# Optimization experiments

Measured on AMD Instinct MI355X. Metric: run time of the kernel, lower is better.

## Reference

```python
import jax, jax.numpy as jnp
from jax import lax
import numpy as np

B, N, C = 4, 2000, 80           # images, proposals/img, foreground classes
SCORE_THR = 0.05
IOU_THR = 0.5
MAX_PER_IMG = 100
K_PRE = 2000                     # pre-NMS top-k candidates per image
STDS = np.array([0.1, 0.1, 0.2, 0.2], dtype=np.float32)
MAX_RATIO = float(abs(np.log(16.0 / 1000.0)))  # wh_ratio_clip=16/1000


def setup_inputs() -> dict:
    key = jax.random.key(0)
    k1, k2, k3 = jax.random.split(key, 3)
    class_outs = jax.random.normal(k1, (B, N, C + 1), dtype=jnp.float32)
    regression_outs = jax.random.normal(k2, (B, N, C * 4), dtype=jnp.float32) * 0.5
    # random valid proposal boxes inside 800x1333 images (x1<x2, y1<y2)
    xy = jax.random.uniform(k3, (B, N, 2, 2), dtype=jnp.float32)
    xy = xy * jnp.array([1333.0, 800.0], dtype=jnp.float32)
    lo = jnp.min(xy, axis=2)
    hi = jnp.max(xy, axis=2) + 1.0
    boxes = jnp.concatenate([lo, hi], axis=-1)  # [B,N,4] x1,y1,x2,y2
    images_hw = jnp.tile(jnp.array([[800, 1333]], dtype=jnp.int32), (B, 1))
    return {"class_outs": class_outs, "regression_outs": regression_outs,
            "boxes": boxes, "images_hw": images_hw}


def _decode(props, deltas, h, w):
    # props [N,4], deltas [N,C,4] -> decoded boxes [N,C,4], clipped to image
    d = deltas * jnp.asarray(STDS)
    dx, dy, dw, dh = d[..., 0], d[..., 1], d[..., 2], d[..., 3]
    dw = jnp.clip(dw, -MAX_RATIO, MAX_RATIO)
    dh = jnp.clip(dh, -MAX_RATIO, MAX_RATIO)
    px = (props[:, None, 0] + props[:, None, 2]) * 0.5
    py = (props[:, None, 1] + props[:, None, 3]) * 0.5
    pw = props[:, None, 2] - props[:, None, 0]
    ph = props[:, None, 3] - props[:, None, 1]
    gx = px + pw * dx
    gy = py + ph * dy
    gw = pw * jnp.exp(dw)
    gh = ph * jnp.exp(dh)
    x1 = jnp.clip(gx - gw * 0.5, 0.0, w)
    y1 = jnp.clip(gy - gh * 0.5, 0.0, h)
    x2 = jnp.clip(gx + gw * 0.5, 0.0, w)
    y2 = jnp.clip(gy + gh * 0.5, 0.0, h)
    return jnp.stack([x1, y1, x2, y2], axis=-1)


def _pairwise_iou(b):
    # b [K,4] -> iou [K,K]
    area = (b[:, 2] - b[:, 0]) * (b[:, 3] - b[:, 1])
    lt = jnp.maximum(b[:, None, :2], b[None, :, :2])
    rb = jnp.minimum(b[:, None, 2:], b[None, :, 2:])
    wh = jnp.clip(rb - lt, 0.0)
    inter = wh[..., 0] * wh[..., 1]
    return inter / (area[:, None] + area[None, :] - inter + 1e-6)


def _process_image(cls_out, reg_out, props, hw):
    h = hw[0].astype(jnp.float32)
    w = hw[1].astype(jnp.float32)
    scores = jax.nn.softmax(cls_out, axis=-1)[:, :C]          # drop background col
    bboxes = _decode(props, reg_out.reshape(N, C, 4), h, w)   # [N,C,4]
    flat_scores = scores.reshape(-1)                          # [N*C]
    flat_boxes = bboxes.reshape(-1, 4)
    labels = jnp.tile(jnp.arange(C, dtype=jnp.int32), N)      # class fastest-varying
    cand = jnp.where(flat_scores > SCORE_THR, flat_scores, -1.0)
    top_scores, top_idx = lax.top_k(cand, K_PRE)
    top_boxes = flat_boxes[top_idx]
    top_labels = labels[top_idx]
    valid = top_scores > SCORE_THR
    # class-offset trick: boxes of distinct classes never overlap
    off = top_labels.astype(jnp.float32)[:, None] * (jnp.maximum(h, w) + 1.0)
    iou = _pairwise_iou(top_boxes + off)                      # [K_PRE,K_PRE]
    idxs = jnp.arange(K_PRE)

    def body(i, keep):
        sup = (idxs > i) & (iou[i] > IOU_THR) & keep[i]
        return keep & ~sup

    keep = lax.fori_loop(0, K_PRE, body, valid)
    kept_scores = jnp.where(keep, top_scores, -1.0)
    det_scores, det_i = lax.top_k(kept_scores, MAX_PER_IMG)
    det_valid = det_scores > SCORE_THR
    det_boxes = jnp.where(det_valid[:, None], top_boxes[det_i], 0.0)
    det_labels = jnp.where(det_valid, top_labels[det_i], -1)
    det_scores = jnp.where(det_valid, det_scores, 0.0)
    return det_boxes, det_scores, det_labels


def reference(class_outs, regression_outs, boxes, images_hw):
    det_boxes, det_scores, det_labels = jax.vmap(_process_image)(
        class_outs, regression_outs, boxes, images_hw)
    return det_boxes, det_scores, det_labels
```

## Files before the change

### kernel.cpp

```cpp
#include <hip/hip_runtime.h>


typedef unsigned long long u64;
typedef unsigned int u32;

#define B_ 4
#define N_ 2000
#define C_ 80
#define NCLS 81
#define KPRE 2000
#define MAXDET 100
#define TARGET 256
#define NB 2312
#define NBPAD 2368
#define NG 37
#define HBASE 0xF500
#define KSHIFT 46
#define CAPA 320
#define CAPB 2048
#define NWAVE 16
#define SEGW 384
#define CAPBLK 128
#define BPI 125
#define BIGI 0x7fffffff

__device__ __forceinline__ u64 pack_key(float score, unsigned fi) {
  return ((u64)__float_as_uint(score) << 32) | (u64)(0xFFFFFFFFu - fi);
}

__device__ __forceinline__ float wred_max(float v) {
  int t;
#define STEPM(ctrl)                                                          \
  t = __builtin_amdgcn_update_dpp(__float_as_int(v), __float_as_int(v),      \
                                  (ctrl), 0xF, 0xF, false);                  \
  v = fmaxf(v, __int_as_float(t));
  STEPM(0x111) STEPM(0x112) STEPM(0x114) STEPM(0x118) STEPM(0x142) STEPM(0x143)
#undef STEPM
  return __int_as_float(__builtin_amdgcn_readlane(__float_as_int(v), 63));
}
__device__ __forceinline__ float wred_sum(float v) {
  int t;
#define STEPS(ctrl)                                                          \
  t = __builtin_amdgcn_update_dpp(0, __float_as_int(v), (ctrl), 0xF, 0xF,    \
                                  false);                                    \
  v = v + __int_as_float(t);
  STEPS(0x111) STEPS(0x112) STEPS(0x114) STEPS(0x118) STEPS(0x142) STEPS(0x143)
#undef STEPS
  return __int_as_float(__builtin_amdgcn_readlane(__float_as_int(v), 63));
}

__device__ __forceinline__ int dpp_min8(int v) {
  int t;
  t = __builtin_amdgcn_update_dpp(BIGI, v, 0x104, 0xF, 0xF, false);
  v = min(v, t);
  t = __builtin_amdgcn_update_dpp(BIGI, v, 0x102, 0xF, 0xF, false);
  v = min(v, t);
  t = __builtin_amdgcn_update_dpp(BIGI, v, 0x101, 0xF, 0xF, false);
  v = min(v, t);
  return v;
}

__device__ __forceinline__ float4 decode_one(
    u64 kk, const float* __restrict__ reg, const float* __restrict__ props,
    int b, float h, float w, float offscale) {
  const float MAXR = 4.135166556742356f;
  unsigned fi = 0xFFFFFFFFu - (u32)kk;
  int n = (int)(fi / (unsigned)C_);
  int c = (int)(fi - (unsigned)n * (unsigned)C_);
  float4 p = ((const float4*)props)[b * N_ + n];
  const float* dl = reg + ((size_t)(b * N_ + n)) * (C_ * 4) + c * 4;
  float dx = dl[0] * 0.1f;
  float dy = dl[1] * 0.1f;
  float dw = fminf(fmaxf(dl[2] * 0.2f, -MAXR), MAXR);
  float dh = fminf(fmaxf(dl[3] * 0.2f, -MAXR), MAXR);
  float px = (p.x + p.z) * 0.5f, py = (p.y + p.w) * 0.5f;
  float pw = p.z - p.x, ph = p.w - p.y;
  float gx = px + pw * dx, gy = py + ph * dy;
  float gw = pw * expf(dw), gh = ph * expf(dh);
  float off = (float)c * offscale;
  return make_float4(fminf(fmaxf(gx - gw * 0.5f, 0.0f), w) + off,
                     fminf(fmaxf(gy - gh * 0.5f, 0.0f), h) + off,
                     fminf(fmaxf(gx + gw * 0.5f, 0.0f), w) + off,
                     fminf(fmaxf(gy + gh * 0.5f, 0.0f), h) + off);
}

__global__ __launch_bounds__(1024) void cand_kernel(
    const float* __restrict__ cls, u64* __restrict__ gkeys, int* __restrict__ gcnt) {
  __shared__ int s_wc[16], s_woff[16];
  const int tid = threadIdx.x;
  const int w = tid >> 6, lane = tid & 63;
  const int blk = blockIdx.x;
  const int b = blk / BPI;
  const int n = (blk % BPI) * 16 + w;
  const float* lg = cls + (size_t)(b * N_ + n) * NCLS;
  float x0 = lg[lane];
  float x1 = (lane < 17) ? lg[64 + lane] : -3.0e38f;
  float mx = wred_max(fmaxf(x0, x1));
  float e0 = expf(x0 - mx);
  float e1 = (lane < 17) ? expf(x1 - mx) : 0.0f;
  float sum = wred_sum(e0 + e1);
  float sc0 = e0 / sum, sc1 = e1 / sum;
  bool p0 = sc0 > 0.05f;
  bool p1 = (lane < 16) && (sc1 > 0.05f);
  u64 m0 = __ballot(p0), m1 = __ballot(p1);
  int c0 = __popcll(m0);
  if (lane == 0) s_wc[w] = c0 + __popcll(m1);
  __syncthreads();
  if (tid == 0) {
    int acc = 0;
#pragma unroll
    for (int i = 0; i < 16; ++i) { s_woff[i] = acc; acc += s_wc[i]; }
    gcnt[blk] = acc;
  }
  __syncthreads();
  const int base = s_woff[w];
  const u64 lt = (1ull << lane) - 1;
  u64* gk = gkeys + (size_t)blk * CAPBLK;
  if (p0) {
    int slot = base + __popcll(m0 & lt);
    if (slot < CAPBLK) gk[slot] = pack_key(sc0, (unsigned)(n * C_ + lane));
  }
  if (p1) {
    int slot = base + c0 + __popcll(m1 & lt);
    if (slot < CAPBLK) gk[slot] = pack_key(sc1, (unsigned)(n * C_ + 64 + lane));
  }
}

__global__ __launch_bounds__(1024) void nmsA_kernel(
    const float* __restrict__ reg, const float* __restrict__ props,
    const int* __restrict__ hw, const u64* __restrict__ gkeys,
    const int* __restrict__ gcnt, int* __restrict__ gflag,
    float* __restrict__ out) {
  __shared__ u64 lds8[7952];
  char* bp = (char*)lds8;
  u64* keylist = (u64*)bp;
  u64* SS = (u64*)bp;
  u64* rb = (u64*)(bp + 8192);
  u32* hist = (u32*)(bp + 49152);
  float4* bxA = (float4*)(bp + 49152);
  u64* U = (u64*)(bp + 58624);
  int* outl = (int*)(bp + 62720);
  int* misc = (int*)(bp + 63232);
  int* segc = (int*)(bp + 63296);
  int* s_coarse = (int*)(bp + 63360);

  const int b = blockIdx.x, tid = threadIdx.x;
  const int wv = tid >> 6, lane = tid & 63;

  float h = (float)hw[b * 2 + 0];
  float w = (float)hw[b * 2 + 1];
  float offscale = fmaxf(h, w) + 1.0f;

  if (tid < 16) misc[tid] = 0;
  if (tid < 64) s_coarse[tid] = 0;
  for (int i = tid; i < NBPAD; i += 1024) hist[i] = 0;
  __syncthreads();

  {
    int cnts[8];
#pragma unroll
    for (int k = 0; k < 8; k++) {
      int p = wv + 16 * k;
      cnts[k] = (p < BPI) ? gcnt[b * BPI + p] : 0;
    }
    bool ovf = false;
    int segoff = 0;
#pragma unroll
    for (int k = 0; k < 8; k++) {
      int p = wv + 16 * k;
      if (p >= BPI) break;
      int cnt = cnts[k];
      if (cnt > CAPBLK) { ovf = true; cnt = CAPBLK; }
      const u64* seg = gkeys + (size_t)(b * BPI + p) * CAPBLK;
#pragma unroll
      for (int r = 0; r < 2; r++) {
        int idx = lane + 64 * r;
        if (idx < cnt) {
          u64 key = seg[idx];
          int bi = min(max((int)(key >> KSHIFT) - HBASE, 0), NB - 1);
          atomicAdd(&hist[bi], 1u);
          int slot = segoff + idx;
          if (slot < SEGW) keylist[wv * SEGW + slot] = key;
        }
      }
      segoff += cnt;
    }
    if (segoff > SEGW) ovf = true;
    if (lane == 0) {
      segc[wv] = min(segoff, SEGW);
      if (ovf) misc[7] = 1;
    }
  }
  __syncthreads();

  for (int g2 = wv; g2 < NG; g2 += NWAVE) {
    int v = (int)hist[(g2 << 6) | lane];
#pragma unroll
    for (int o = 32; o; o >>= 1) v += __shfl_xor(v, o);
    if (lane == 0) s_coarse[g2] = v;
  }
  __syncthreads();

  if (tid < 64) {
    int v = s_coarse[lane];
#pragma unroll
    for (int off = 1; off < 64; off <<= 1) {
      int src = lane + off;
      int o = __shfl(v, src < 64 ? src : 63);
      if (src < 64) v += o;
    }
    int Mtot = __shfl(v, 0);
    u64 pm = __ballot(v >= TARGET);
    int T_A = 0, S_A;
    if (pm) {
      int gs = 63 - __builtin_clzll(pm);
      int beyond = __shfl(v, gs + 1);
      int fv = (int)hist[(gs << 6) | lane];
#pragma unroll
      for (int off = 1; off < 64; off <<= 1) {
        int src = lane + off;
        int o = __shfl(fv, src < 64 ? src : 63);
        if (src < 64) fv += o;
      }
      int cum = beyond + fv;
      u64 pm2 = __ballot(cum >= TARGET);
      int tr = 63 - __builtin_clzll(pm2);
      T_A = (gs << 6) + tr;
      S_A = __shfl(cum, tr);
    } else {
      S_A = Mtot;
    }
    if (lane == 0) { misc[0] = T_A; misc[2] = S_A; misc[3] = Mtot; misc[4] = 0; }
  }
  __syncthreads();

  int T_A = misc[0], S_A = misc[2], Mtot = misc[3];
  bool modeB = (S_A > CAPA) || (misc[7] != 0);
  int K = 0, nkept = 0;

  if (!modeB) {
    for (int s = 0; s < NWAVE; s++) {
      int Mg = segc[s];
      bool pred = false;
      u64 key = 0;
      if (tid < Mg) {
        key = keylist[s * SEGW + tid];
        int bi = min(max((int)(key >> KSHIFT) - HBASE, 0), NB - 1);
        pred = (bi >= T_A);
      }
      u64 mk = __ballot(pred);
      if (mk) {
        int wbase = 0;
        if (lane == 0) wbase = atomicAdd(&misc[4], __popcll(mk));
        wbase = __shfl(wbase, 0);
        if (pred) {
          int pos = wbase + __popcll(mk & ((1ull << lane) - 1));
          if (pos < CAPA) U[pos] = key;
        }
      }
    }
    __syncthreads();
    int S = misc[4];
    if (S > CAPA) S = CAPA;
    if (tid == 0 && (S & 1)) U[S] = 0ULL;
    __syncthreads();
    if (tid < S) {
      u64 k1 = U[tid];
      int r1 = 0;
      const ulonglong2* Uu2 = (const ulonglong2*)U;
      int half = (S + 1) >> 1;
      for (int k = 0; k < half; k++) {
        ulonglong2 kk = Uu2[k];
        r1 += (kk.x > k1) + (kk.y > k1);
      }
      SS[r1] = k1;
    }
    __syncthreads();
    K = S;
    for (int j = tid; j < K; j += 1024)
      bxA[j] = decode_one(SS[j], reg, props, b, h, w, offscale);
    __syncthreads();

    int nwords = (S + 63) >> 6;
    int ntiles = nwords * (nwords + 1) / 2;
    for (int t = wv; t < ntiles; t += NWAVE) {
      int ti = 0, rem = t;
      while (rem >= nwords - ti) { rem -= nwords - ti; ti++; }
      int tj = ti + rem;
      int i = (ti << 6) + lane;
      float4 bi4 = bxA[i];
      float ai = (bi4.z - bi4.x) * (bi4.w - bi4.y);
      u64 bits = 0;
      int jbase = tj << 6;
      int jcount = min(64, S - jbase);
      for (int jj = 0; jj < jcount; jj++) {
        int j = jbase + jj;
        float4 bj = bxA[j];
        float aj = (bj.z - bj.x) * (bj.w - bj.y);
        float iw = fmaxf(fminf(bi4.z, bj.z) - fmaxf(bi4.x, bj.x), 0.0f);
        float ih = fmaxf(fminf(bi4.w, bj.w) - fmaxf(bi4.y, bj.y), 0.0f);
        float inter = iw * ih;
        float iou = inter / (ai + aj - inter + 1e-6f);
        if (j > i && iou > 0.5f) bits |= (1ull << jj);
      }
      if (i < S) rb[i * 8 + tj] = bits;
    }
    __syncthreads();

    if (tid < 64) {
      u64 alive = 0;
      if (lane < nwords) {
        alive = ~0ull;
        int remb = S & 63;
        if (lane == nwords - 1 && remb) alive = (1ull << remb) - 1;
      }
      int nk = 0;
      if (S > 0) {
        int i = 0;
        u64 row = (lane < nwords) ? rb[0 * 8 + lane] : 0ull;
        for (;;) {
          if (lane == 0) outl[nk] = i;
          nk++;
          if (nk >= MAXDET) break;
          if (lane == (i >> 6)) alive &= ~(1ull << (i & 63));
          u64 rowSpec = (i + 1 < S && lane < nwords) ? rb[(i + 1) * 8 + lane] : 0ull;
          u64 a2 = alive & ~row;
          alive = a2;
          int cnd = a2 ? ((lane << 6) + (int)__builtin_ctzll(a2)) : BIGI;
          int m8 = dpp_min8(cnd);
          int ni = __builtin_amdgcn_readfirstlane(m8);
          if (ni >= BIGI) break;
          row = (ni == i + 1) ? rowSpec
                              : ((lane < nwords) ? rb[ni * 8 + lane] : 0ull);
          i = ni;
        }
      }
      if (lane == 0) misc[6] = nk;
    }
    __syncthreads();
    nkept = misc[6];
    if (nkept < MAXDET && K < Mtot && K < KPRE) modeB = true;
  }

  if (tid == 0) gflag[b] = modeB ? 1 : 0;
  if (modeB) return;

  float* oBox = out;
  float* oSc = out + B_ * MAXDET * 4;
  float* oLb = out + B_ * MAXDET * 5;
  for (int k2 = tid; k2 < MAXDET; k2 += 1024) {
    float4 bb = make_float4(0.0f, 0.0f, 0.0f, 0.0f);
    float sv = 0.0f, lv = -1.0f;
    if (k2 < nkept) {
      int idx = outl[k2];
      u64 kk = SS[idx];
      sv = __uint_as_float((u32)(kk >> 32));
      unsigned fi = 0xFFFFFFFFu - (u32)kk;
      int c = (int)(fi % (unsigned)C_);
      float off = (float)c * offscale;
      float4 ob = bxA[idx];
      bb = make_float4(ob.x - off, ob.y - off, ob.z - off, ob.w - off);
      lv = (float)c;
    }
    oBox[(b * MAXDET + k2) * 4 + 0] = bb.x;
    oBox[(b * MAXDET + k2) * 4 + 1] = bb.y;
    oBox[(b * MAXDET + k2) * 4 + 2] = bb.z;
    oBox[(b * MAXDET + k2) * 4 + 3] = bb.w;
    oSc[b * MAXDET + k2] = sv;
    oLb[b * MAXDET + k2] = lv;
  }
}

__global__ __launch_bounds__(1024) void nmsB_kernel(
    const float* __restrict__ reg, const float* __restrict__ props,
    const int* __restrict__ hw, const u64* __restrict__ gkeys,
    const int* __restrict__ gcnt, const int* __restrict__ gflag,
    float* __restrict__ out) {
  const int b = blockIdx.x, tid = threadIdx.x;
  if (gflag[b] == 0) return;

  __shared__ u64 lds8[7952];
  char* bp = (char*)lds8;
  u32* hist = (u32*)(bp + 0);
  u64* U2 = (u64*)(bp + 9472);
  u64* SSB = (u64*)(bp + 25856);
  int* outl = (int*)(bp + 42240);
  int* misc = (int*)(bp + 42752);
  const int wv = tid >> 6, lane = tid & 63;

  float h = (float)hw[b * 2 + 0];
  float w = (float)hw[b * 2 + 1];
  float offscale = fmaxf(h, w) + 1.0f;

  for (int i = tid; i < NBPAD; i += 1024) hist[i] = 0;
  if (tid < 16) misc[tid] = 0;
  __syncthreads();

  for (int k = 0; k < 8; k++) {
    int p = wv + 16 * k;
    if (p >= BPI) break;
    int cnt = min(gcnt[b * BPI + p], CAPBLK);
    const u64* seg = gkeys + (size_t)(b * BPI + p) * CAPBLK;
#pragma unroll
    for (int r = 0; r < 2; r++) {
      int idx = lane + 64 * r;
      if (idx < cnt) {
        u64 key = seg[idx];
        int bi = min(max((int)(key >> KSHIFT) - HBASE, 0), NB - 1);
        atomicAdd(&hist[bi], 1u);
      }
    }
  }
  __syncthreads();

  if (tid == 0) {
    int acc = 0, tb = 0;
    for (int bi = NB - 1; bi >= 0; bi--) {
      acc += (int)hist[bi];
      if (acc >= KPRE) { tb = bi; break; }
    }
    if (acc > CAPB) tb = min(tb + 1, NB - 1);
    misc[1] = tb;
    misc[4] = 0;
  }
  __syncthreads();
  int T_B = misc[1];

  for (int k = 0; k < 8; k++) {
    int p = wv + 16 * k;
    if (p >= BPI) break;
    int cnt = min(gcnt[b * BPI + p], CAPBLK);
    const u64* seg = gkeys + (size_t)(b * BPI + p) * CAPBLK;
#pragma unroll
    for (int r = 0; r < 2; r++) {
      int idx = lane + 64 * r;
      bool pred = false;
      u64 key = 0;
      if (idx < cnt) {
        key = seg[idx];
        int bi = min(max((int)(key >> KSHIFT) - HBASE, 0), NB - 1);
        pred = (bi >= T_B);
      }
      u64 mk = __ballot(pred);
      if (mk) {
        int wbase = 0;
        if (lane == 0) wbase = atomicAdd(&misc[4], __popcll(mk));
        wbase = __shfl(wbase, 0);
        if (pred) {
          int pos = wbase + __popcll(mk & ((1ull << lane) - 1));
          if (pos < CAPB) U2[pos] = key;
        }
      }
    }
  }
  __syncthreads();
  int S = misc[4];
  if (S > CAPB) S = CAPB;
  {
    int j1 = tid, j2 = tid + 1024;
    u64 k1 = (j1 < S) ? U2[j1] : 0ULL;
    u64 k2 = (j2 < S) ? U2[j2] : 0ULL;
    int r1 = 0, r2 = 0;
    for (int k = 0; k < S; k++) {
      u64 kk = U2[k];
// ... 51 lines not shown
      i = ni;
    }
  }
  if (tid == 0) misc[6] = nk;
  __syncthreads();
  int nkept = misc[6];

  float* oBox = out;
  float* oSc = out + B_ * MAXDET * 4;
  float* oLb = out + B_ * MAXDET * 5;
  for (int k2 = tid; k2 < MAXDET; k2 += 1024) {
    float4 bb = make_float4(0.0f, 0.0f, 0.0f, 0.0f);
    float sv = 0.0f, lv = -1.0f;
    if (k2 < nkept) {
      int idx = outl[k2];
      u64 kk = SSB[idx];
      sv = __uint_as_float((u32)(kk >> 32));
      unsigned fi = 0xFFFFFFFFu - (u32)kk;
      int c = (int)(fi % (unsigned)C_);
      float off = (float)c * offscale;
      float4 ob = decode_one(kk, reg, props, b, h, w, offscale);
      bb = make_float4(ob.x - off, ob.y - off, ob.z - off, ob.w - off);
      lv = (float)c;
    }
    oBox[(b * MAXDET + k2) * 4 + 0] = bb.x;
    oBox[(b * MAXDET + k2) * 4 + 1] = bb.y;
    oBox[(b * MAXDET + k2) * 4 + 2] = bb.z;
    oBox[(b * MAXDET + k2) * 4 + 3] = bb.w;
    oSc[b * MAXDET + k2] = sv;
    oLb[b * MAXDET + k2] = lv;
  }
}

extern "C" void kernel_launch(void* const* d_in, const int* in_sizes, int n_in,
                              void* d_out, int out_size, void* d_ws, size_t ws_size,
                              hipStream_t stream) {
  const float* cls = (const float*)d_in[0];
  const float* reg = (const float*)d_in[1];
  const float* props = (const float*)d_in[2];
  const int* hw = (const int*)d_in[3];
  float* out = (float*)d_out;

  int* gcnt = (int*)d_ws;
  u64* gkeys = (u64*)((char*)d_ws + 2048);
  int* gflag = (int*)((char*)d_ws + 514048);

  cand_kernel<<<B_ * BPI, 1024, 0, stream>>>(cls, gkeys, gcnt);
  nmsA_kernel<<<B_, 1024, 0, stream>>>(reg, props, hw, gkeys, gcnt, gflag, out);
  nmsB_kernel<<<B_, 1024, 0, stream>>>(reg, props, hw, gkeys, gcnt, gflag, out);
}
```

Baseline: 107.1 us.

## Fuse candidate, NMS-A and NMS-B kernels into one launch with flag spin-wait

Merges the candidate-scoring kernel and both NMS kernels into a single launch. Every block writes its candidate keys and then publishes its count with a magic-tagged release store. The first B blocks go on to do NMS, spin-waiting with acquire loads on each producer's flag, and call a noinline cold path instead of a separate fallback kernel. This removes two kernel launches and their gaps. The risks are inter-block spin dependencies that rely on all blocks being scheduled, and tagged flags left in the workspace from earlier calls that are never cleared, so a later call may read stale counts.

```diff
diff --git a/kernel.cpp b/kernel.cpp
--- a/kernel.cpp
+++ b/kernel.cpp
@@ -23,6 +23,7 @@
 #define CAPBLK 128
 #define BPI 125
 #define BIGI 0x7fffffff
+#define MAGIC 0x5EC7u
 
 __device__ __forceinline__ u64 pack_key(float score, unsigned fi) {
   return ((u64)__float_as_uint(score) << 32) | (u64)(0xFFFFFFFFu - fi);
@@ -84,313 +85,17 @@
                      fminf(fmaxf(gy + gh * 0.5f, 0.0f), h) + off);
 }
 
-__global__ __launch_bounds__(1024) void cand_kernel(
-    const float* __restrict__ cls, u64* __restrict__ gkeys, int* __restrict__ gcnt) {
-  __shared__ int s_wc[16], s_woff[16];
-  const int tid = threadIdx.x;
-  const int w = tid >> 6, lane = tid & 63;
-  const int blk = blockIdx.x;
-  const int b = blk / BPI;
-  const int n = (blk % BPI) * 16 + w;
-  const float* lg = cls + (size_t)(b * N_ + n) * NCLS;
-  float x0 = lg[lane];
-  float x1 = (lane < 17) ? lg[64 + lane] : -3.0e38f;
-  float mx = wred_max(fmaxf(x0, x1));
-  float e0 = expf(x0 - mx);
-  float e1 = (lane < 17) ? expf(x1 - mx) : 0.0f;
-  float sum = wred_sum(e0 + e1);
-  float sc0 = e0 / sum, sc1 = e1 / sum;
-  bool p0 = sc0 > 0.05f;
-  bool p1 = (lane < 16) && (sc1 > 0.05f);
-  u64 m0 = __ballot(p0), m1 = __ballot(p1);
-  int c0 = __popcll(m0);
-  if (lane == 0) s_wc[w] = c0 + __popcll(m1);
-  __syncthreads();
-  if (tid == 0) {
-    int acc = 0;
-#pragma unroll
-    for (int i = 0; i < 16; ++i) { s_woff[i] = acc; acc += s_wc[i]; }
-    gcnt[blk] = acc;
-  }
-  __syncthreads();
-  const int base = s_woff[w];
-  const u64 lt = (1ull << lane) - 1;
-  u64* gk = gkeys + (size_t)blk * CAPBLK;
-  if (p0) {
-    int slot = base + __popcll(m0 & lt);
-    if (slot < CAPBLK) gk[slot] = pack_key(sc0, (unsigned)(n * C_ + lane));
-  }
-  if (p1) {
-    int slot = base + c0 + __popcll(m1 & lt);
-    if (slot < CAPBLK) gk[slot] = pack_key(sc1, (unsigned)(n * C_ + 64 + lane));
-  }
-}
-
-__global__ __launch_bounds__(1024) void nmsA_kernel(
-    const float* __restrict__ reg, const float* __restrict__ props,
-    const int* __restrict__ hw, const u64* __restrict__ gkeys,
-    const int* __restrict__ gcnt, int* __restrict__ gflag,
-    float* __restrict__ out) {
-  __shared__ u64 lds8[7952];
-  char* bp = (char*)lds8;
-  u64* keylist = (u64*)bp;
-  u64* SS = (u64*)bp;
-  u64* rb = (u64*)(bp + 8192);
-  u32* hist = (u32*)(bp + 49152);
-  float4* bxA = (float4*)(bp + 49152);
-  u64* U = (u64*)(bp + 58624);
-  int* outl = (int*)(bp + 62720);
-  int* misc = (int*)(bp + 63232);
-  int* segc = (int*)(bp + 63296);
-  int* s_coarse = (int*)(bp + 63360);
-
-  const int b = blockIdx.x, tid = threadIdx.x;
-  const int wv = tid >> 6, lane = tid & 63;
-
-  float h = (float)hw[b * 2 + 0];
-  float w = (float)hw[b * 2 + 1];
-  float offscale = fmaxf(h, w) + 1.0f;
-
-  if (tid < 16) misc[tid] = 0;
-  if (tid < 64) s_coarse[tid] = 0;
-  for (int i = tid; i < NBPAD; i += 1024) hist[i] = 0;
-  __syncthreads();
-
-  {
-    int cnts[8];
-#pragma unroll
-    for (int k = 0; k < 8; k++) {
-      int p = wv + 16 * k;
-      cnts[k] = (p < BPI) ? gcnt[b * BPI + p] : 0;
-    }
-    bool ovf = false;
-    int segoff = 0;
-#pragma unroll
-    for (int k = 0; k < 8; k++) {
-      int p = wv + 16 * k;
-      if (p >= BPI) break;
-      int cnt = cnts[k];
-      if (cnt > CAPBLK) { ovf = true; cnt = CAPBLK; }
-      const u64* seg = gkeys + (size_t)(b * BPI + p) * CAPBLK;
-#pragma unroll
-      for (int r = 0; r < 2; r++) {
-        int idx = lane + 64 * r;
-        if (idx < cnt) {
-          u64 key = seg[idx];
-          int bi = min(max((int)(key >> KSHIFT) - HBASE, 0), NB - 1);
-          atomicAdd(&hist[bi], 1u);
-          int slot = segoff + idx;
-          if (slot < SEGW) keylist[wv * SEGW + slot] = key;
-        }
-      }
-      segoff += cnt;
-    }
-    if (segoff > SEGW) ovf = true;
-    if (lane == 0) {
-      segc[wv] = min(segoff, SEGW);
-      if (ovf) misc[7] = 1;
-    }
-  }
-  __syncthreads();
-
-  for (int g2 = wv; g2 < NG; g2 += NWAVE) {
-    int v = (int)hist[(g2 << 6) | lane];
-#pragma unroll
-    for (int o = 32; o; o >>= 1) v += __shfl_xor(v, o);
-    if (lane == 0) s_coarse[g2] = v;
-  }
-  __syncthreads();
-
-  if (tid < 64) {
-    int v = s_coarse[lane];
-#pragma unroll
-    for (int off = 1; off < 64; off <<= 1) {
-      int src = lane + off;
-      int o = __shfl(v, src < 64 ? src : 63);
-      if (src < 64) v += o;
-    }
-    int Mtot = __shfl(v, 0);
-    u64 pm = __ballot(v >= TARGET);
-    int T_A = 0, S_A;
-    if (pm) {
-      int gs = 63 - __builtin_clzll(pm);
-      int beyond = __shfl(v, gs + 1);
-      int fv = (int)hist[(gs << 6) | lane];
-#pragma unroll
-      for (int off = 1; off < 64; off <<= 1) {
-        int src = lane + off;
-        int o = __shfl(fv, src < 64 ? src : 63);
-        if (src < 64) fv += o;
-      }
-      int cum = beyond + fv;
-      u64 pm2 = __ballot(cum >= TARGET);
-      int tr = 63 - __builtin_clzll(pm2);
-      T_A = (gs << 6) + tr;
-      S_A = __shfl(cum, tr);
-    } else {
-      S_A = Mtot;
-    }
-    if (lane == 0) { misc[0] = T_A; misc[2] = S_A; misc[3] = Mtot; misc[4] = 0; }
-  }
-  __syncthreads();
-
-  int T_A = misc[0], S_A = misc[2], Mtot = misc[3];
-  bool modeB = (S_A > CAPA) || (misc[7] != 0);
-  int K = 0, nkept = 0;
-
-  if (!modeB) {
-    for (int s = 0; s < NWAVE; s++) {
-      int Mg = segc[s];
-      bool pred = false;
-      u64 key = 0;
-      if (tid < Mg) {
-        key = keylist[s * SEGW + tid];
-        int bi = min(max((int)(key >> KSHIFT) - HBASE, 0), NB - 1);
-        pred = (bi >= T_A);
-      }
-      u64 mk = __ballot(pred);
-      if (mk) {
-        int wbase = 0;
-        if (lane == 0) wbase = atomicAdd(&misc[4], __popcll(mk));
-        wbase = __shfl(wbase, 0);
-        if (pred) {
-          int pos = wbase + __popcll(mk & ((1ull << lane) - 1));
-          if (pos < CAPA) U[pos] = key;
-        }
-      }
-    }
-    __syncthreads();
-    int S = misc[4];
-    if (S > CAPA) S = CAPA;
-    if (tid == 0 && (S & 1)) U[S] = 0ULL;
-    __syncthreads();
-    if (tid < S) {
-      u64 k1 = U[tid];
-      int r1 = 0;
-      const ulonglong2* Uu2 = (const ulonglong2*)U;
-      int half = (S + 1) >> 1;
-      for (int k = 0; k < half; k++) {
-        ulonglong2 kk = Uu2[k];
-        r1 += (kk.x > k1) + (kk.y > k1);
-      }
-      SS[r1] = k1;
-    }
-    __syncthreads();
-    K = S;
-    for (int j = tid; j < K; j += 1024)
-      bxA[j] = decode_one(SS[j], reg, props, b, h, w, offscale);
-    __syncthreads();
-
-    int nwords = (S + 63) >> 6;
-    int ntiles = nwords * (nwords + 1) / 2;
-    for (int t = wv; t < ntiles; t += NWAVE) {
-      int ti = 0, rem = t;
-      while (rem >= nwords - ti) { rem -= nwords - ti; ti++; }
-      int tj = ti + rem;
-      int i = (ti << 6) + lane;
-      float4 bi4 = bxA[i];
-      float ai = (bi4.z - bi4.x) * (bi4.w - bi4.y);
-      u64 bits = 0;
-      int jbase = tj << 6;
-      int jcount = min(64, S - jbase);
-      for (int jj = 0; jj < jcount; jj++) {
-        int j = jbase + jj;
-        float4 bj = bxA[j];
-        float aj = (bj.z - bj.x) * (bj.w - bj.y);
-        float iw = fmaxf(fminf(bi4.z, bj.z) - fmaxf(bi4.x, bj.x), 0.0f);
-        float ih = fmaxf(fminf(bi4.w, bj.w) - fmaxf(bi4.y, bj.y), 0.0f);
-        float inter = iw * ih;
-        float iou = inter / (ai + aj - inter + 1e-6f);
-        if (j > i && iou > 0.5f) bits |= (1ull << jj);
-      }
-      if (i < S) rb[i * 8 + tj] = bits;
-    }
-    __syncthreads();
-
-    if (tid < 64) {
-      u64 alive = 0;
-      if (lane < nwords) {
-        alive = ~0ull;
-        int remb = S & 63;
-        if (lane == nwords - 1 && remb) alive = (1ull << remb) - 1;
-      }
-      int nk = 0;
-      if (S > 0) {
-        int i = 0;
-        u64 row = (lane < nwords) ? rb[0 * 8 + lane] : 0ull;
-        for (;;) {
-          if (lane == 0) outl[nk] = i;
-          nk++;
-          if (nk >= MAXDET) break;
-          if (lane == (i >> 6)) alive &= ~(1ull << (i & 63));
-          u64 rowSpec = (i + 1 < S && lane < nwords) ? rb[(i + 1) * 8 + lane] : 0ull;
-          u64 a2 = alive & ~row;
-          alive = a2;
-          int cnd = a2 ? ((lane << 6) + (int)__builtin_ctzll(a2)) : BIGI;
-          int m8 = dpp_min8(cnd);
-          int ni = __builtin_amdgcn_readfirstlane(m8);
-          if (ni >= BIGI) break;
-          row = (ni == i + 1) ? rowSpec
-                              : ((lane < nwords) ? rb[ni * 8 + lane] : 0ull);
-          i = ni;
-        }
-      }
-      if (lane == 0) misc[6] = nk;
-    }
-    __syncthreads();
-    nkept = misc[6];
-    if (nkept < MAXDET && K < Mtot && K < KPRE) modeB = true;
-  }
-
-  if (tid == 0) gflag[b] = modeB ? 1 : 0;
-  if (modeB) return;
-
-  float* oBox = out;
-  float* oSc = out + B_ * MAXDET * 4;
-  float* oLb = out + B_ * MAXDET * 5;
-  for (int k2 = tid; k2 < MAXDET; k2 += 1024) {
-    float4 bb = make_float4(0.0f, 0.0f, 0.0f, 0.0f);
-    float sv = 0.0f, lv = -1.0f;
-    if (k2 < nkept) {
-      int idx = outl[k2];
-      u64 kk = SS[idx];
-      sv = __uint_as_float((u32)(kk >> 32));
-      unsigned fi = 0xFFFFFFFFu - (u32)kk;
-      int c = (int)(fi % (unsigned)C_);
-      float off = (float)c * offscale;
-      float4 ob = bxA[idx];
-      bb = make_float4(ob.x - off, ob.y - off, ob.z - off, ob.w - off);
-      lv = (float)c;
-    }
-    oBox[(b * MAXDET + k2) * 4 + 0] = bb.x;
-    oBox[(b * MAXDET + k2) * 4 + 1] = bb.y;
-    oBox[(b * MAXDET + k2) * 4 + 2] = bb.z;
-    oBox[(b * MAXDET + k2) * 4 + 3] = bb.w;
-    oSc[b * MAXDET + k2] = sv;
-    oLb[b * MAXDET + k2] = lv;
-  }
-}
-
-__global__ __launch_bounds__(1024) void nmsB_kernel(
-    const float* __restrict__ reg, const float* __restrict__ props,
-    const int* __restrict__ hw, const u64* __restrict__ gkeys,
-    const int* __restrict__ gcnt, const int* __restrict__ gflag,
-    float* __restrict__ out) {
-  const int b = blockIdx.x, tid = threadIdx.x;
-  if (gflag[b] == 0) return;
-
-  __shared__ u64 lds8[7952];
-  char* bp = (char*)lds8;
+__device__ __noinline__ static void nmsB_cold(
+    char* bp, const float* __restrict__ reg, const float* __restrict__ props,
+    const u64* __restrict__ gkeys, const u32* __restrict__ gcnt,
+    float* __restrict__ out, int b, float h, float w, float offscale) {
   u32* hist = (u32*)(bp + 0);
   u64* U2 = (u64*)(bp + 9472);
   u64* SSB = (u64*)(bp + 25856);
   int* outl = (int*)(bp + 42240);
   int* misc = (int*)(bp + 42752);
+  const int tid = threadIdx.x;
   const int wv = tid >> 6, lane = tid & 63;
-
-  float h = (float)hw[b * 2 + 0];
-  float w = (float)hw[b * 2 + 1];
-  float offscale = fmaxf(h, w) + 1.0f;
 
   for (int i = tid; i < NBPAD; i += 1024) hist[i] = 0;
   if (tid < 16) misc[tid] = 0;
@@ -399,7 +104,7 @@
   for (int k = 0; k < 8; k++) {
     int p = wv + 16 * k;
     if (p >= BPI) break;
-    int cnt = min(gcnt[b * BPI + p], CAPBLK);
+    int cnt = min((int)(gcnt[b * BPI + p] & 0xFFFFu), CAPBLK);
     const u64* seg = gkeys + (size_t)(b * BPI + p) * CAPBLK;
 #pragma unroll
     for (int r = 0; r < 2; r++) {
@@ -429,7 +134,7 @@
   for (int k = 0; k < 8; k++) {
     int p = wv + 16 * k;
     if (p >= BPI) break;
-    int cnt = min(gcnt[b * BPI + p], CAPBLK);
+    int cnt = min((int)(gcnt[b * BPI + p] & 0xFFFFu), CAPBLK);
     const u64* seg = gkeys + (size_t)(b * BPI + p) * CAPBLK;
 #pragma unroll
     for (int r = 0; r < 2; r++) {
@@ -547,6 +252,303 @@
   }
 }
 
+__global__ __launch_bounds__(1024) void fused_kernel(
+    const float* __restrict__ cls, const float* __restrict__ reg,
+    const float* __restrict__ props, const int* __restrict__ hw,
+    u64* __restrict__ gkeys, u32* __restrict__ gcnt, float* __restrict__ out) {
+  __shared__ u64 lds8[7976];
+  char* bp = (char*)lds8;
+  u64* keylist = (u64*)bp;
+  u64* SS = (u64*)bp;
+  u64* rb = (u64*)(bp + 8192);
+  u32* hist = (u32*)(bp + 49152);
+  float4* bxA = (float4*)(bp + 49152);
+  u64* U = (u64*)(bp + 58624);
+  int* outl = (int*)(bp + 62720);
+  int* misc = (int*)(bp + 63232);
+  int* segc = (int*)(bp + 63296);
+  int* s_coarse = (int*)(bp + 63360);
+  int* s_wc = (int*)(bp + 63616);
+  int* s_woff = (int*)(bp + 63680);
+
+  const int tid = threadIdx.x;
+  const int wv = tid >> 6, lane = tid & 63;
+
+  {
+    const int blk = blockIdx.x;
+    const int pb = blk / BPI;
+    const int n = (blk % BPI) * 16 + wv;
+    const float* lg = cls + (size_t)(pb * N_ + n) * NCLS;
+    float x0 = lg[lane];
+    float x1 = (lane < 17) ? lg[64 + lane] : -3.0e38f;
+    float mx = wred_max(fmaxf(x0, x1));
+    float e0 = expf(x0 - mx);
+    float e1 = (lane < 17) ? expf(x1 - mx) : 0.0f;
+    float sum = wred_sum(e0 + e1);
+    float sc0 = e0 / sum, sc1 = e1 / sum;
+    bool p0 = sc0 > 0.05f;
+    bool p1 = (lane < 16) && (sc1 > 0.05f);
+    u64 m0 = __ballot(p0), m1 = __ballot(p1);
+    int c0 = __popcll(m0);
+    if (lane == 0) s_wc[wv] = c0 + __popcll(m1);
+    __syncthreads();
+    int acc_keep = 0;
+    if (tid == 0) {
+      int acc = 0;
+#pragma unroll
+      for (int i = 0; i < 16; ++i) { s_woff[i] = acc; acc += s_wc[i]; }
+      acc_keep = acc;
+    }
+    __syncthreads();
+    const int base = s_woff[wv];
+    const u64 lt = (1ull << lane) - 1;
+    u64* gk = gkeys + (size_t)blk * CAPBLK;
+    if (p0) {
+      int slot = base + __popcll(m0 & lt);
+      if (slot < CAPBLK) gk[slot] = pack_key(sc0, (unsigned)(n * C_ + lane));
+    }
+    if (p1) {
+      int slot = base + c0 + __popcll(m1 & lt);
+      if (slot < CAPBLK) gk[slot] = pack_key(sc1, (unsigned)(n * C_ + 64 + lane));
+    }
+    __syncthreads();
+    if (tid == 0) {
+      __threadfence();
+      __hip_atomic_store(&gcnt[blk], (u32)acc_keep | (MAGIC << 16),
+                         __ATOMIC_RELEASE, __HIP_MEMORY_SCOPE_AGENT);
+    }
+  }
+
+  const int b = blockIdx.x;
+  if (b >= B_) return;
+
+  if (tid < 16) misc[tid] = 0;
+  if (tid < 64) s_coarse[tid] = 0;
+  for (int i = tid; i < NBPAD; i += 1024) hist[i] = 0;
+  float h = (float)hw[b * 2 + 0];
+  float w = (float)hw[b * 2 + 1];
+  float offscale = fmaxf(h, w) + 1.0f;
+  __syncthreads();
+
+  {
+    bool ovf = false;
+    int segoff = 0;
+    for (int k = 0; k < 8; k++) {
+      int p = wv + 16 * k;
+      if (p >= BPI) break;
+      u32 v = 0;
+      if (lane == 0) {
+        do {
+          v = __hip_atomic_load(&gcnt[b * BPI + p], __ATOMIC_ACQUIRE,
+                                __HIP_MEMORY_SCOPE_AGENT);
+        } while ((v >> 16) != MAGIC);
+      }
+      v = (u32)__shfl((int)v, 0);
+      int cnt = (int)(v & 0xFFFFu);
+      if (cnt > CAPBLK) { ovf = true; cnt = CAPBLK; }
+      const u64* seg = gkeys + (size_t)(b * BPI + p) * CAPBLK;
+#pragma unroll
+      for (int r = 0; r < 2; r++) {
+        int idx = lane + 64 * r;
+        if (idx < cnt) {
+          u64 key = seg[idx];
+          int bi = min(max((int)(key >> KSHIFT) - HBASE, 0), NB - 1);
+          atomicAdd(&hist[bi], 1u);
+          int slot = segoff + idx;
+          if (slot < SEGW) keylist[wv * SEGW + slot] = key;
+        }
+      }
+      segoff += cnt;
+    }
+    if (segoff > SEGW) ovf = true;
+    if (lane == 0) {
+      segc[wv] = min(segoff, SEGW);
+      if (ovf) misc[7] = 1;
+    }
+  }
+  __syncthreads();
+
+  for (int g2 = wv; g2 < NG; g2 += NWAVE) {
+    int v = (int)hist[(g2 << 6) | lane];
+#pragma unroll
+    for (int o = 32; o; o >>= 1) v += __shfl_xor(v, o);
+    if (lane == 0) s_coarse[g2] = v;
+  }
+  __syncthreads();
+
+  if (tid < 64) {
+    int v = s_coarse[lane];
+#pragma unroll
+    for (int off = 1; off < 64; off <<= 1) {
+      int src = lane + off;
+      int o = __shfl(v, src < 64 ? src : 63);
+      if (src < 64) v += o;
+    }
+    int Mtot = __shfl(v, 0);
+    u64 pm = __ballot(v >= TARGET);
+    int T_A = 0, S_A;
+    if (pm) {
+      int gs = 63 - __builtin_clzll(pm);
+      int beyond = __shfl(v, gs + 1);
+      int fv = (int)hist[(gs << 6) | lane];
+#pragma unroll
+      for (int off = 1; off < 64; off <<= 1) {
+        int src = lane + off;
+        int o = __shfl(fv, src < 64 ? src : 63);
+        if (src < 64) fv += o;
+      }
+      int cum = beyond + fv;
+      u64 pm2 = __ballot(cum >= TARGET);
+      int tr = 63 - __builtin_clzll(pm2);
+      T_A = (gs << 6) + tr;
+      S_A = __shfl(cum, tr);
+    } else {
+      S_A = Mtot;
+    }
+    if (lane == 0) { misc[0] = T_A; misc[2] = S_A; misc[3] = Mtot; misc[4] = 0; }
+  }
+  __syncthreads();
+
+  int T_A = misc[0], S_A = misc[2], Mtot = misc[3];
+  bool modeB = (S_A > CAPA) || (misc[7] != 0);
+  int K = 0, nkept = 0;
+
+  if (!modeB) {
+    for (int s = 0; s < NWAVE; s++) {
+      int Mg = segc[s];
+      bool pred = false;
+      u64 key = 0;
+      if (tid < Mg) {
+        key = keylist[s * SEGW + tid];
+        int bi = min(max((int)(key >> KSHIFT) - HBASE, 0), NB - 1);
+        pred = (bi >= T_A);
+      }
+      u64 mk = __ballot(pred);
+      if (mk) {
+        int wbase = 0;
+        if (lane == 0) wbase = atomicAdd(&misc[4], __popcll(mk));
+        wbase = __shfl(wbase, 0);
+        if (pred) {
+          int pos = wbase + __popcll(mk & ((1ull << lane) - 1));
+          if (pos < CAPA) U[pos] = key;
+        }
+      }
+    }
+    __syncthreads();
+    int S = misc[4];
+    if (S > CAPA) S = CAPA;
+    if (tid == 0 && (S & 1)) U[S] = 0ULL;
+    __syncthreads();
+    if (tid < S) {
+      u64 k1 = U[tid];
+      int r1 = 0;
+      const ulonglong2* Uu2 = (const ulonglong2*)U;
+      int half = (S + 1) >> 1;
+      for (int k = 0; k < half; k++) {
+        ulonglong2 kk = Uu2[k];
+        r1 += (kk.x > k1) + (kk.y > k1);
+      }
+      SS[r1] = k1;
+    }
+    __syncthreads();
+    K = S;
+    for (int j = tid; j < K; j += 1024)
+      bxA[j] = decode_one(SS[j], reg, props, b, h, w, offscale);
+    __syncthreads();
+
+    int nwords = (S + 63) >> 6;
+    int ntiles = nwords * (nwords + 1) / 2;
+    for (int t = wv; t < ntiles; t += NWAVE) {
+      int ti = 0, rem = t;
+      while (rem >= nwords - ti) { rem -= nwords - ti; ti++; }
+      int tj = ti + rem;
+      int i = (ti << 6) + lane;
+      float4 bi4 = bxA[i];
+      float ai = (bi4.z - bi4.x) * (bi4.w - bi4.y);
+      u64 bits = 0;
+      int jbase = tj << 6;
+      int jcount = min(64, S - jbase);
+      for (int jj = 0; jj < jcount; jj++) {
+        int j = jbase + jj;
+        float4 bj = bxA[j];
+        float aj = (bj.z - bj.x) * (bj.w - bj.y);
+        float iw = fmaxf(fminf(bi4.z, bj.z) - fmaxf(bi4.x, bj.x), 0.0f);
+        float ih = fmaxf(fminf(bi4.w, bj.w) - fmaxf(bi4.y, bj.y), 0.0f);
+        float inter = iw * ih;
+        float iou = inter / (ai + aj - inter + 1e-6f);
+        if (j > i && iou > 0.5f) bits |= (1ull << jj);
+      }
+      if (i < S) rb[i * 8 + tj] = bits;
+    }
+    __syncthreads();
+
+    if (tid < 64) {
+      int nwords7 = (S + 63) >> 6;
+      u64 alive = 0;
+      if (lane < nwords7) {
+        alive = ~0ull;
+        int remb = S & 63;
+        if (lane == nwords7 - 1 && remb) alive = (1ull << remb) - 1;
+      }
+      int nk = 0;
+      if (S > 0) {
+        int i = 0;
+        u64 row = (lane < nwords7) ? rb[0 * 8 + lane] : 0ull;
+        for (;;) {
+          if (lane == 0) outl[nk] = i;
+          nk++;
+          if (nk >= MAXDET) break;
+          if (lane == (i >> 6)) alive &= ~(1ull << (i & 63));
+          u64 rowSpec = (i + 1 < S && lane < nwords7) ? rb[(i + 1) * 8 + lane] : 0ull;
+          u64 a2 = alive & ~row;
+          alive = a2;
+          int cnd = a2 ? ((lane << 6) + (int)__builtin_ctzll(a2)) : BIGI;
+          int m8 = dpp_min8(cnd);
+          int ni = __builtin_amdgcn_readfirstlane(m8);
+          if (ni >= BIGI) break;
+          row = (ni == i + 1) ? rowSpec
+                              : ((lane < nwords7) ? rb[ni * 8 + lane] : 0ull);
+          i = ni;
+        }
+      }
+      if (lane == 0) misc[6] = nk;
+    }
+    __syncthreads();
+    nkept = misc[6];
+    if (nkept < MAXDET && K < Mtot && K < KPRE) modeB = true;
+  }
+
+  if (modeB) {
+    nmsB_cold(bp, reg, props, gkeys, gcnt, out, b, h, w, offscale);
+    return;
+  }
+
+  float* oBox = out;
+  float* oSc = out + B_ * MAXDET * 4;
+  float* oLb = out + B_ * MAXDET * 5;
+  for (int k2 = tid; k2 < MAXDET; k2 += 1024) {
+    float4 bb = make_float4(0.0f, 0.0f, 0.0f, 0.0f);
+    float sv = 0.0f, lv = -1.0f;
+    if (k2 < nkept) {
+      int idx = outl[k2];
+      u64 kk = SS[idx];
+      sv = __uint_as_float((u32)(kk >> 32));
+      unsigned fi = 0xFFFFFFFFu - (u32)kk;
+      int c = (int)(fi % (unsigned)C_);
+      float off = (float)c * offscale;
+      float4 ob = bxA[idx];
+      bb = make_float4(ob.x - off, ob.y - off, ob.z - off, ob.w - off);
+      lv = (float)c;
+    }
+    oBox[(b * MAXDET + k2) * 4 + 0] = bb.x;
+    oBox[(b * MAXDET + k2) * 4 + 1] = bb.y;
+    oBox[(b * MAXDET + k2) * 4 + 2] = bb.z;
+    oBox[(b * MAXDET + k2) * 4 + 3] = bb.w;
+    oSc[b * MAXDET + k2] = sv;
+    oLb[b * MAXDET + k2] = lv;
+  }
+}
+
 extern "C" void kernel_launch(void* const* d_in, const int* in_sizes, int n_in,
                               void* d_out, int out_size, void* d_ws, size_t ws_size,
                               hipStream_t stream) {
@@ -556,11 +558,9 @@
   const int* hw = (const int*)d_in[3];
   float* out = (float*)d_out;
 
-  int* gcnt = (int*)d_ws;
+  u32* gcnt = (u32*)d_ws;
   u64* gkeys = (u64*)((char*)d_ws + 2048);
-  int* gflag = (int*)((char*)d_ws + 514048);
-
-  cand_kernel<<<B_ * BPI, 1024, 0, stream>>>(cls, gkeys, gcnt);
-  nmsA_kernel<<<B_, 1024, 0, stream>>>(reg, props, hw, gkeys, gcnt, gflag, out);
-  nmsB_kernel<<<B_, 1024, 0, stream>>>(reg, props, hw, gkeys, gcnt, gflag, out);
-}
+
+  fused_kernel<<<B_ * BPI, 1024, 0, stream>>>(cls, reg, props, hw,
+                                              gkeys, gcnt, out);
+}
```

Result: slower. 134.5 us (+25.6%).

## Build score histogram in candidate kernel and split threshold into separate kernel

Applied to the files above, without the earlier changes.

The per-image score histogram is now built with global atomics inside the 500-block candidate kernel instead of being rebuilt inside the 4-block NMS kernel. A new small thresh_kernel turns that histogram into the top-k bucket threshold. nmsA then makes a single pass over the keys to filter them, with no staging keylist and a smaller shared-memory footprint. This moves serial work off the few-block NMS stage, at the cost of an extra memset, an extra kernel launch and contended global atomics.

```diff
diff --git a/kernel.cpp b/kernel.cpp
--- a/kernel.cpp
+++ b/kernel.cpp
@@ -18,14 +18,21 @@
 #define KSHIFT 46
 #define CAPA 320
 #define CAPB 2048
-#define NWAVE 16
-#define SEGW 384
 #define CAPBLK 128
 #define BPI 125
 #define BIGI 0x7fffffff
 
+#define WS_GCNT  0
+#define WS_GKEYS 2048
+#define WS_GFLAG 514048
+#define WS_GTHR  514064
+#define WS_GHIST 514112
+
 __device__ __forceinline__ u64 pack_key(float score, unsigned fi) {
   return ((u64)__float_as_uint(score) << 32) | (u64)(0xFFFFFFFFu - fi);
+}
+__device__ __forceinline__ int bucket_of_bits(u32 sb) {
+  return min(max((int)(sb >> 14) - HBASE, 0), NB - 1);
 }
 
 __device__ __forceinline__ float wred_max(float v) {
@@ -85,7 +92,8 @@
 }
 
 __global__ __launch_bounds__(1024) void cand_kernel(
-    const float* __restrict__ cls, u64* __restrict__ gkeys, int* __restrict__ gcnt) {
+    const float* __restrict__ cls, u64* __restrict__ gkeys,
+    int* __restrict__ gcnt, u32* __restrict__ ghist) {
   __shared__ int s_wc[16], s_woff[16];
   const int tid = threadIdx.x;
   const int w = tid >> 6, lane = tid & 63;
@@ -116,91 +124,35 @@
   const int base = s_woff[w];
   const u64 lt = (1ull << lane) - 1;
   u64* gk = gkeys + (size_t)blk * CAPBLK;
+  u32* gh = ghist + (size_t)b * NBPAD;
   if (p0) {
     int slot = base + __popcll(m0 & lt);
     if (slot < CAPBLK) gk[slot] = pack_key(sc0, (unsigned)(n * C_ + lane));
+    atomicAdd(&gh[bucket_of_bits(__float_as_uint(sc0))], 1u);
   }
   if (p1) {
     int slot = base + c0 + __popcll(m1 & lt);
     if (slot < CAPBLK) gk[slot] = pack_key(sc1, (unsigned)(n * C_ + 64 + lane));
-  }
-}
-
-__global__ __launch_bounds__(1024) void nmsA_kernel(
-    const float* __restrict__ reg, const float* __restrict__ props,
-    const int* __restrict__ hw, const u64* __restrict__ gkeys,
-    const int* __restrict__ gcnt, int* __restrict__ gflag,
-    float* __restrict__ out) {
-  __shared__ u64 lds8[7952];
-  char* bp = (char*)lds8;
-  u64* keylist = (u64*)bp;
-  u64* SS = (u64*)bp;
-  u64* rb = (u64*)(bp + 8192);
-  u32* hist = (u32*)(bp + 49152);
-  float4* bxA = (float4*)(bp + 49152);
-  u64* U = (u64*)(bp + 58624);
-  int* outl = (int*)(bp + 62720);
-  int* misc = (int*)(bp + 63232);
-  int* segc = (int*)(bp + 63296);
-  int* s_coarse = (int*)(bp + 63360);
-
+    atomicAdd(&gh[bucket_of_bits(__float_as_uint(sc1))], 1u);
+  }
+}
+
+__global__ __launch_bounds__(1024) void thresh_kernel(
+    const u32* __restrict__ ghist, int* __restrict__ gthr) {
+  __shared__ u32 hist[NBPAD];
+  __shared__ int s_coarse[64];
   const int b = blockIdx.x, tid = threadIdx.x;
   const int wv = tid >> 6, lane = tid & 63;
-
-  float h = (float)hw[b * 2 + 0];
-  float w = (float)hw[b * 2 + 1];
-  float offscale = fmaxf(h, w) + 1.0f;
-
-  if (tid < 16) misc[tid] = 0;
+  for (int i = tid; i < NBPAD; i += 1024) hist[i] = ghist[b * NBPAD + i];
   if (tid < 64) s_coarse[tid] = 0;
-  for (int i = tid; i < NBPAD; i += 1024) hist[i] = 0;
-  __syncthreads();
-
-  {
-    int cnts[8];
-#pragma unroll
-    for (int k = 0; k < 8; k++) {
-      int p = wv + 16 * k;
-      cnts[k] = (p < BPI) ? gcnt[b * BPI + p] : 0;
-    }
-    bool ovf = false;
-    int segoff = 0;
-#pragma unroll
-    for (int k = 0; k < 8; k++) {
-      int p = wv + 16 * k;
-      if (p >= BPI) break;
-      int cnt = cnts[k];
-      if (cnt > CAPBLK) { ovf = true; cnt = CAPBLK; }
-      const u64* seg = gkeys + (size_t)(b * BPI + p) * CAPBLK;
-#pragma unroll
-      for (int r = 0; r < 2; r++) {
-        int idx = lane + 64 * r;
-        if (idx < cnt) {
-          u64 key = seg[idx];
-          int bi = min(max((int)(key >> KSHIFT) - HBASE, 0), NB - 1);
-          atomicAdd(&hist[bi], 1u);
-          int slot = segoff + idx;
-          if (slot < SEGW) keylist[wv * SEGW + slot] = key;
-        }
-      }
-      segoff += cnt;
-    }
-    if (segoff > SEGW) ovf = true;
-    if (lane == 0) {
-      segc[wv] = min(segoff, SEGW);
-      if (ovf) misc[7] = 1;
-    }
-  }
-  __syncthreads();
-
-  for (int g2 = wv; g2 < NG; g2 += NWAVE) {
+  __syncthreads();
+  for (int g2 = wv; g2 < NG; g2 += 16) {
     int v = (int)hist[(g2 << 6) | lane];
 #pragma unroll
     for (int o = 32; o; o >>= 1) v += __shfl_xor(v, o);
     if (lane == 0) s_coarse[g2] = v;
   }
   __syncthreads();
-
   if (tid < 64) {
     int v = s_coarse[lane];
 #pragma unroll
@@ -230,116 +182,166 @@
     } else {
       S_A = Mtot;
     }
-    if (lane == 0) { misc[0] = T_A; misc[2] = S_A; misc[3] = Mtot; misc[4] = 0; }
-  }
-  __syncthreads();
-
-  int T_A = misc[0], S_A = misc[2], Mtot = misc[3];
-  bool modeB = (S_A > CAPA) || (misc[7] != 0);
+    if (lane == 0) {
+      gthr[b * 4 + 0] = T_A;
+      gthr[b * 4 + 1] = S_A;
+      gthr[b * 4 + 2] = Mtot;
+    }
+  }
+}
+
+__global__ __launch_bounds__(1024) void nmsA_kernel(
+    const float* __restrict__ reg, const float* __restrict__ props,
+    const int* __restrict__ hw, const u64* __restrict__ gkeys,
+    const int* __restrict__ gcnt, const int* __restrict__ gthr,
+    int* __restrict__ gflag, float* __restrict__ out) {
+  __shared__ u64 lds8[4106];
+  char* bp = (char*)lds8;
+  u64* SS = (u64*)bp;
+  u64* rb = (u64*)(bp + 4096);
+  float4* bxA = (float4*)(bp + 24576);
+  u64* U = (u64*)(bp + 29696);
+  int* outl = (int*)(bp + 32272);
+  int* misc = (int*)(bp + 32784);
+
+  const int b = blockIdx.x, tid = threadIdx.x;
+  const int wv = tid >> 6, lane = tid & 63;
+
+  float h = (float)hw[b * 2 + 0];
+  float w = (float)hw[b * 2 + 1];
+  float offscale = fmaxf(h, w) + 1.0f;
+  const int T_A = gthr[b * 4 + 0];
+  const int S_A = gthr[b * 4 + 1];
+  const int Mtot = gthr[b * 4 + 2];
+
+  if (tid < 16) misc[tid] = 0;
+  __syncthreads();
+
+  bool modeB = (S_A > CAPA);
   int K = 0, nkept = 0;
 
   if (!modeB) {
-    for (int s = 0; s < NWAVE; s++) {
-      int Mg = segc[s];
-      bool pred = false;
-      u64 key = 0;
-      if (tid < Mg) {
-        key = keylist[s * SEGW + tid];
-        int bi = min(max((int)(key >> KSHIFT) - HBASE, 0), NB - 1);
-        pred = (bi >= T_A);
-      }
-      u64 mk = __ballot(pred);
-      if (mk) {
-        int wbase = 0;
-        if (lane == 0) wbase = atomicAdd(&misc[4], __popcll(mk));
-        wbase = __shfl(wbase, 0);
-        if (pred) {
-          int pos = wbase + __popcll(mk & ((1ull << lane) - 1));
-          if (pos < CAPA) U[pos] = key;
-        }
-      }
-    }
+    int cnts[8];
+#pragma unroll
+    for (int k = 0; k < 8; k++) {
+      int p = wv + 16 * k;
+      cnts[k] = (p < BPI) ? gcnt[b * BPI + p] : 0;
+    }
+    bool ovf = false;
+#pragma unroll
+    for (int k = 0; k < 8; k++) {
+      int p = wv + 16 * k;
+      if (p >= BPI) break;
+      int cnt = cnts[k];
+      if (cnt > CAPBLK) { ovf = true; cnt = CAPBLK; }
+      const u64* seg = gkeys + (size_t)(b * BPI + p) * CAPBLK;
+#pragma unroll
+      for (int r = 0; r < 2; r++) {
+        int idx = lane + 64 * r;
+        bool pred = false;
+        u64 key = 0;
+        if (idx < cnt) {
+          key = seg[idx];
+          pred = (bucket_of_bits((u32)(key >> 32)) >= T_A);
+        }
+        u64 mk = __ballot(pred);
+        if (mk) {
+          int wbase = 0;
+          if (lane == 0) wbase = atomicAdd(&misc[4], __popcll(mk));
+          wbase = __shfl(wbase, 0);
+          if (pred) {
+            int pos = wbase + __popcll(mk & ((1ull << lane) - 1));
+            if (pos < CAPA) U[pos] = key;
+          }
+        }
+      }
+    }
+    if (lane == 0 && ovf) misc[7] = 1;
     __syncthreads();
+    if (misc[7]) modeB = true;
     int S = misc[4];
     if (S > CAPA) S = CAPA;
-    if (tid == 0 && (S & 1)) U[S] = 0ULL;
-    __syncthreads();
-    if (tid < S) {
-      u64 k1 = U[tid];
-      int r1 = 0;
-      const ulonglong2* Uu2 = (const ulonglong2*)U;
-      int half = (S + 1) >> 1;
-      for (int k = 0; k < half; k++) {
-        ulonglong2 kk = Uu2[k];
-        r1 += (kk.x > k1) + (kk.y > k1);
-      }
-      SS[r1] = k1;
-    }
-    __syncthreads();
-    K = S;
-    for (int j = tid; j < K; j += 1024)
-      bxA[j] = decode_one(SS[j], reg, props, b, h, w, offscale);
-    __syncthreads();
-
-    int nwords = (S + 63) >> 6;
-    int ntiles = nwords * (nwords + 1) / 2;
-    for (int t = wv; t < ntiles; t += NWAVE) {
-      int ti = 0, rem = t;
-      while (rem >= nwords - ti) { rem -= nwords - ti; ti++; }
-      int tj = ti + rem;
-      int i = (ti << 6) + lane;
-      float4 bi4 = bxA[i];
-      float ai = (bi4.z - bi4.x) * (bi4.w - bi4.y);
-      u64 bits = 0;
-      int jbase = tj << 6;
-      int jcount = min(64, S - jbase);
-      for (int jj = 0; jj < jcount; jj++) {
-        int j = jbase + jj;
-        float4 bj = bxA[j];
-        float aj = (bj.z - bj.x) * (bj.w - bj.y);
-        float iw = fmaxf(fminf(bi4.z, bj.z) - fmaxf(bi4.x, bj.x), 0.0f);
-        float ih = fmaxf(fminf(bi4.w, bj.w) - fmaxf(bi4.y, bj.y), 0.0f);
-        float inter = iw * ih;
-        float iou = inter / (ai + aj - inter + 1e-6f);
-        if (j > i && iou > 0.5f) bits |= (1ull << jj);
-      }
-      if (i < S) rb[i * 8 + tj] = bits;
-    }
-    __syncthreads();
-
-    if (tid < 64) {
-      u64 alive = 0;
-      if (lane < nwords) {
-        alive = ~0ull;
-        int remb = S & 63;
-        if (lane == nwords - 1 && remb) alive = (1ull << remb) - 1;
-      }
-      int nk = 0;
-      if (S > 0) {
-        int i = 0;
-        u64 row = (lane < nwords) ? rb[0 * 8 + lane] : 0ull;
-        for (;;) {
-          if (lane == 0) outl[nk] = i;
-          nk++;
-          if (nk >= MAXDET) break;
-          if (lane == (i >> 6)) alive &= ~(1ull << (i & 63));
-          u64 rowSpec = (i + 1 < S && lane < nwords) ? rb[(i + 1) * 8 + lane] : 0ull;
-          u64 a2 = alive & ~row;
-          alive = a2;
-          int cnd = a2 ? ((lane << 6) + (int)__builtin_ctzll(a2)) : BIGI;
-          int m8 = dpp_min8(cnd);
-          int ni = __builtin_amdgcn_readfirstlane(m8);
-          if (ni >= BIGI) break;
-          row = (ni == i + 1) ? rowSpec
-                              : ((lane < nwords) ? rb[ni * 8 + lane] : 0ull);
-          i = ni;
-        }
-      }
-      if (lane == 0) misc[6] = nk;
-    }
-    __syncthreads();
-    nkept = misc[6];
-    if (nkept < MAXDET && K < Mtot && K < KPRE) modeB = true;
+
+    if (!modeB) {
+      if (tid == 0 && (S & 1)) U[S] = 0ULL;
+      __syncthreads();
+      if (tid < S) {
+        u64 k1 = U[tid];
+        int r1 = 0;
+        const ulonglong2* Uu2 = (const ulonglong2*)U;
+        int half = (S + 1) >> 1;
+        for (int k = 0; k < half; k++) {
+          ulonglong2 kk = Uu2[k];
+          r1 += (kk.x > k1) + (kk.y > k1);
+        }
+        SS[r1] = k1;
+      }
+      __syncthreads();
+      K = S;
+      for (int j = tid; j < K; j += 1024)
+        bxA[j] = decode_one(SS[j], reg, props, b, h, w, offscale);
+      __syncthreads();
+
+      int nwords = (S + 63) >> 6;
+      int ntiles = nwords * (nwords + 1) / 2;
+      for (int t = wv; t < ntiles; t += 16) {
+        int ti = 0, rem = t;
+        while (rem >= nwords - ti) { rem -= nwords - ti; ti++; }
+        int tj = ti + rem;
+        int i = (ti << 6) + lane;
+        float4 bi4 = bxA[i];
+        float ai = (bi4.z - bi4.x) * (bi4.w - bi4.y);
+        u64 bits = 0;
+        int jbase = tj << 6;
+        int jcount = min(64, S - jbase);
+        for (int jj = 0; jj < jcount; jj++) {
+          int j = jbase + jj;
+          float4 bj = bxA[j];
+          float aj = (bj.z - bj.x) * (bj.w - bj.y);
+          float iw = fmaxf(fminf(bi4.z, bj.z) - fmaxf(bi4.x, bj.x), 0.0f);
+          float ih = fmaxf(fminf(bi4.w, bj.w) - fmaxf(bi4.y, bj.y), 0.0f);
+          float inter = iw * ih;
+          float iou = inter / (ai + aj - inter + 1e-6f);
+          if (j > i && iou > 0.5f) bits |= (1ull << jj);
+        }
+        if (i < S) rb[i * 8 + tj] = bits;
+      }
+      __syncthreads();
+
+      if (tid < 64) {
+        u64 alive = 0;
+        if (lane < nwords) {
+          alive = ~0ull;
+          int remb = S & 63;
+          if (lane == nwords - 1 && remb) alive = (1ull << remb) - 1;
+        }
+        int nk = 0;
+        if (S > 0) {
+          int i = 0;
+          u64 row = (lane < nwords) ? rb[0 * 8 + lane] : 0ull;
+          for (;;) {
+            if (lane == 0) outl[nk] = i;
+            nk++;
+            if (nk >= MAXDET) break;
+            if (lane == (i >> 6)) alive &= ~(1ull << (i & 63));
+            u64 rowSpec = (i + 1 < S && lane < nwords) ? rb[(i + 1) * 8 + lane] : 0ull;
+            u64 a2 = alive & ~row;
+            alive = a2;
+            int cnd = a2 ? ((lane << 6) + (int)__builtin_ctzll(a2)) : BIGI;
+            int m8 = dpp_min8(cnd);
+            int ni = __builtin_amdgcn_readfirstlane(m8);
+            if (ni >= BIGI) break;
+            row = (ni == i + 1) ? rowSpec
+                                : ((lane < nwords) ? rb[ni * 8 + lane] : 0ull);
+            i = ni;
+          }
+        }
+        if (lane == 0) misc[6] = nk;
+      }
+      __syncthreads();
+      nkept = misc[6];
+      if (nkept < MAXDET && K < Mtot && K < KPRE) modeB = true;
+    }
   }
 
   if (tid == 0) gflag[b] = modeB ? 1 : 0;
@@ -556,11 +558,16 @@
   const int* hw = (const int*)d_in[3];
   float* out = (float*)d_out;
 
-  int* gcnt = (int*)d_ws;
-  u64* gkeys = (u64*)((char*)d_ws + 2048);
-  int* gflag = (int*)((char*)d_ws + 514048);
-
-  cand_kernel<<<B_ * BPI, 1024, 0, stream>>>(cls, gkeys, gcnt);
-  nmsA_kernel<<<B_, 1024, 0, stream>>>(reg, props, hw, gkeys, gcnt, gflag, out);
+  int* gcnt = (int*)((char*)d_ws + WS_GCNT);
+  u64* gkeys = (u64*)((char*)d_ws + WS_GKEYS);
+  int* gflag = (int*)((char*)d_ws + WS_GFLAG);
+  int* gthr = (int*)((char*)d_ws + WS_GTHR);
+  u32* ghist = (u32*)((char*)d_ws + WS_GHIST);
+
+  hipMemsetAsync(ghist, 0, (size_t)B_ * NBPAD * 4, stream);
+  cand_kernel<<<B_ * BPI, 1024, 0, stream>>>(cls, gkeys, gcnt, ghist);
+  thresh_kernel<<<B_, 1024, 0, stream>>>(ghist, gthr);
+  nmsA_kernel<<<B_, 1024, 0, stream>>>(reg, props, hw, gkeys, gcnt, gthr,
+                                       gflag, out);
   nmsB_kernel<<<B_, 1024, 0, stream>>>(reg, props, hw, gkeys, gcnt, gflag, out);
 }
```

Result: slower. 112.3 us (+4.9%).
